# Kernel optimization log

Measured on AMD Instinct MI355X. Metric: run time of the kernel, lower is better.

Reference implementation:

```python
import jax, jax.numpy as jnp
import numpy as np

N_NODES = 50000
N_EDGES = 800000
EPS = 0.1

def setup_inputs() -> dict:
    key = jax.random.key(0)
    ks = jax.random.split(key, 6)
    x = jax.random.normal(ks[0], (N_NODES, 256), dtype=jnp.float32)
    edge_index = jax.random.randint(ks[1], (2, N_EDGES), 0, N_NODES, dtype=jnp.int64)
    W1 = jax.random.normal(ks[2], (256, 64), dtype=jnp.float32) * (1.0 / np.sqrt(256))
    b1 = jnp.zeros((64,), dtype=jnp.float32)
    att = jax.random.normal(ks[3], (2, 1, 64), dtype=jnp.float32) * (1.0 / np.sqrt(64))
    W2 = jax.random.normal(ks[4], (64, 16), dtype=jnp.float32) * (1.0 / np.sqrt(64))
    b2 = jnp.zeros((16,), dtype=jnp.float32)
    return {"x": x, "edge_index": edge_index, "W1": W1, "b1": b1, "att": att, "W2": W2, "b2": b2}

def _fagcn_conv(x, row, col, norm, att_l, eps):
    # message: norm * x_j gathered at source (row), scatter-add to target (col)
    msg = norm[:, None] * x[row]                      # [E_tot, H]
    x_l = jax.ops.segment_sum(msg, col, num_segments=N_NODES)  # low-pass
    x_h = -eps * x_l                                   # high-pass message = -eps * low message
    gate = jax.nn.sigmoid(jnp.sum(x * att_l, axis=-1, keepdims=True))  # [N,1]
    return gate * x_l + (1.0 - gate) * x_h

def reference(x, edge_index, W1, b1, att, W2, b2):
    # add self loops once (same edge set is reused by every layer)
    loops = jnp.arange(N_NODES, dtype=edge_index.dtype)
    row = jnp.concatenate([edge_index[0], loops])
    col = jnp.concatenate([edge_index[1], loops])
    deg = jax.ops.segment_sum(jnp.ones_like(col, dtype=x.dtype), col, num_segments=N_NODES)
    dinv = jnp.where(deg > 0, jax.lax.rsqrt(jnp.maximum(deg, 1e-30)), 0.0)
    norm = dinv[row] * dinv[col]                       # [E_tot]
    # eval mode: dropout is identity
    h = jax.nn.relu(x @ W1 + b1)                       # [N, H]
    for l in range(att.shape[0]):
        h = _fagcn_conv(h, row, col, norm, att[l], EPS)
    return h @ W2 + b2                                 # [N, out]
```

## Files before the change

### kernel.cpp

```cpp
#include <hip/hip_runtime.h>
#include <math.h>

#define N_FEAT_IN 256
#define N_HID 64
#define N_OUT 16
#define EPS 0.1f

typedef short bf16x8 __attribute__((ext_vector_type(8)));
typedef float f32x4 __attribute__((ext_vector_type(4)));

__device__ inline uint pack2(ushort a, ushort b) { return (uint)a | ((uint)b << 16); }

__device__ inline ushort bf16_rne(float x) {
    uint b = __float_as_uint(x);
    b += 0x7fff + ((b >> 16) & 1);
    return (ushort)(b >> 16);
}

__device__ inline float blo(uint u) { return __uint_as_float(u << 16); }
__device__ inline float bhi(uint u) { return __uint_as_float(u & 0xffff0000u); }

__device__ inline void split_bf16(float x, ushort& hi, ushort& lo) {
    uint b = __float_as_uint(x);
    hi = (ushort)(b >> 16);
    float xl = x - __uint_as_float(b & 0xffff0000u);
    lo = (ushort)(__float_as_uint(xl) >> 16);
}


__global__ void zero_int(int* __restrict__ p, int n) {
    int i = blockIdx.x * blockDim.x + threadIdx.x;
    if (i < n) p[i] = 0;
}


__global__ void hist_rank(const int* __restrict__ col, int* __restrict__ cnt,
                          int* __restrict__ rank, int E) {
    int e = blockIdx.x * blockDim.x + threadIdx.x;
    if (e < E) rank[e] = atomicAdd(&cnt[col[e]], 1);
}


__global__ void scan_chunks(const int* __restrict__ cnt, int* __restrict__ rowptr,
                            int* __restrict__ partial, float* __restrict__ dinv, int N) {
    __shared__ int sm[256];
    int tid = threadIdx.x;
    int gid = blockIdx.x * 256 + tid;
    int v = (gid < N) ? cnt[gid] : 0;
    sm[tid] = v;
    __syncthreads();
#pragma unroll
    for (int off = 1; off < 256; off <<= 1) {
        int add = (tid >= off) ? sm[tid - off] : 0;
        __syncthreads();
        sm[tid] += add;
        __syncthreads();
    }
    if (gid < N) {
        rowptr[gid] = sm[tid] - v;
        dinv[gid] = rsqrtf(1.0f + (float)v);
    }
    if (tid == 255) partial[blockIdx.x] = sm[255];
}

__global__ void scan_partials(int* __restrict__ partial, int nchunks) {
    __shared__ int sm[256];
    int tid = threadIdx.x;
    int v = (tid < nchunks) ? partial[tid] : 0;
    sm[tid] = v;
    __syncthreads();
#pragma unroll
    for (int off = 1; off < 256; off <<= 1) {
        int add = (tid >= off) ? sm[tid - off] : 0;
        __syncthreads();
        sm[tid] += add;
        __syncthreads();
    }
    if (tid < nchunks) partial[tid] = sm[tid] - v;
}

__global__ void scan_finish(int* __restrict__ rowptr, const int* __restrict__ partial,
                            int N, int E) {
    int gid = blockIdx.x * 256 + threadIdx.x;
    if (gid < N) rowptr[gid] += partial[blockIdx.x];
    if (gid == 0) rowptr[N] = E;
}


__global__ void csr_scatter_part(const int* __restrict__ row, const int* __restrict__ col,
                                 const int* __restrict__ rank, const int* __restrict__ rowptr,
                                 ushort* __restrict__ srcidx, int E, int rangeSz) {
    int r = blockIdx.x & 7;
    int nsl = gridDim.x >> 3;
    int s = blockIdx.x >> 3;
    int lo = r * rangeSz;
    int hi = lo + rangeSz;
    int stride = nsl * blockDim.x;
    for (int e = s * blockDim.x + threadIdx.x; e < E; e += stride) {
        int c = col[e];
        if (c >= lo && c < hi) {
            srcidx[rowptr[c] + rank[e]] = (ushort)row[e];
        }
    }
}


__global__ __launch_bounds__(256) void gemm1_mfma(const float* __restrict__ x,
                                                  const float* __restrict__ W1,
                                                  const float* __restrict__ b1,
                                                  const float* __restrict__ dinv,
                                                  uint* __restrict__ AsOut,
                                                  int MB, int totalWaves) {
    __shared__ uint4 wh_lds[2048];
    __shared__ uint4 wl_lds[2048];
    int tid = threadIdx.x;
    for (int e = tid; e < 2048; e += 256) {
        int ks = e >> 8;
        int rem = e & 255;
        int nt = rem >> 6;
        int ln = rem & 63;
        int k0 = ks * 32 + ((ln >> 4) << 3);
        int colw = nt * 16 + (ln & 15);
        ushort hi[8], lo[8];
#pragma unroll
        for (int i = 0; i < 8; ++i) {
            float v = W1[(k0 + i) * 64 + colw];
            split_bf16(v, hi[i], lo[i]);
        }
        wh_lds[e] = make_uint4(pack2(hi[0], hi[1]), pack2(hi[2], hi[3]),
                               pack2(hi[4], hi[5]), pack2(hi[6], hi[7]));
        wl_lds[e] = make_uint4(pack2(lo[0], lo[1]), pack2(lo[2], lo[3]),
                               pack2(lo[4], lo[5]), pack2(lo[6], lo[7]));
    }
    __syncthreads();

    int lane = tid & 63;
    int m = lane & 15;
    int kg = lane >> 4;
    int wid = blockIdx.x * 4 + (tid >> 6);
    const bf16x8* whf = reinterpret_cast<const bf16x8*>(wh_lds);
    const bf16x8* wlf = reinterpret_cast<const bf16x8*>(wl_lds);
    float bias[4];
#pragma unroll
    for (int nt = 0; nt < 4; ++nt) bias[nt] = b1[nt * 16 + m];

    auto load_tile = [&](float4* dst, int mbv) {
        const float4* xr = reinterpret_cast<const float4*>(x) +
                           (size_t)(mbv * 16 + m) * 64 + kg * 2;
#pragma unroll
        for (int ks = 0; ks < 8; ++ks) {
            dst[2 * ks]     = xr[ks * 8];
            dst[2 * ks + 1] = xr[ks * 8 + 1];
        }
    };

    int mb = wid;
    if (mb >= MB) return;
    float4 xv[16], xn[16];
    load_tile(xv, mb);

    while (true) {
        int mbn = mb + totalWaves;
        bool has_next = (mbn < MB);
        if (has_next) load_tile(xn, mbn);

        f32x4 acc[4] = {{0.f,0.f,0.f,0.f},{0.f,0.f,0.f,0.f},
                        {0.f,0.f,0.f,0.f},{0.f,0.f,0.f,0.f}};
#pragma unroll
        for (int ks = 0; ks < 8; ++ks) {
            float4 a0 = xv[2 * ks];
            float4 a1 = xv[2 * ks + 1];
            float f[8] = {a0.x, a0.y, a0.z, a0.w, a1.x, a1.y, a1.z, a1.w};
            bf16x8 ah, al;
#pragma unroll
            for (int i = 0; i < 8; ++i) {
                ushort hu, lu;
                split_bf16(f[i], hu, lu);
                ah[i] = (short)hu;
                al[i] = (short)lu;
            }
#pragma unroll
            for (int nt = 0; nt < 4; ++nt) {
                bf16x8 wh = whf[(ks * 4 + nt) * 64 + lane];
                bf16x8 wl = wlf[(ks * 4 + nt) * 64 + lane];
                acc[nt] = __builtin_amdgcn_mfma_f32_16x16x32_bf16(ah, wh, acc[nt], 0, 0, 0);
                acc[nt] = __builtin_amdgcn_mfma_f32_16x16x32_bf16(al, wh, acc[nt], 0, 0, 0);
                acc[nt] = __builtin_amdgcn_mfma_f32_16x16x32_bf16(ah, wl, acc[nt], 0, 0, 0);
            }
        }

        int r0 = mb * 16 + kg * 4;
        float dr[4];
#pragma unroll
        for (int j = 0; j < 4; ++j) dr[j] = dinv[r0 + j];
#pragma unroll
        for (int nt = 0; nt < 4; ++nt) {
#pragma unroll
            for (int j = 0; j < 4; ++j) {
                float v = fmaxf(acc[nt][j] + bias[nt], 0.0f) * dr[j];
                float p = __shfl_xor(v, 1, 64);
                if ((m & 1) == 0) {
                    uint u = pack2(bf16_rne(v), bf16_rne(p));
                    AsOut[(size_t)(r0 + j) * 32 + ((nt * 16 + m) >> 1)] = u;
                }
            }
        }

        if (!has_next) break;
#pragma unroll
        for (int u = 0; u < 16; ++u) xv[u] = xn[u];
        mb = mbn;
    }
}


template <bool LAST>
__global__ __launch_bounds__(256) void fagcn_layer(
    const uint2* __restrict__ As2, uint2* __restrict__ Out2,
    const float* __restrict__ dinv, const int* __restrict__ rowptr,
    const ushort* __restrict__ src, const float* __restrict__ att_l,
    const float* __restrict__ W2, const float* __restrict__ b2,
    float* __restrict__ out, int N) {
    __shared__ float W2s[64 * 16];
    __shared__ float hL[16 * 68];
    int tid = threadIdx.x;
    if (LAST) {
        for (int e = tid; e < 64 * 16; e += 256) W2s[e] = W2[e];
        __syncthreads();
    }
    int sub = tid & 15;
    int lnode = tid >> 4;
    int i = blockIdx.x * 16 + lnode;
    if (i >= N) i = N - 1;

    int start = rowptr[i];
    int end = rowptr[i + 1];
    uint2 su = As2[(size_t)i * 16 + sub];
    float self0 = blo(su.x), self1 = bhi(su.x);
    float self2 = blo(su.y), self3 = bhi(su.y);

    float aA0 = 0.f, aA1 = 0.f, aA2 = 0.f, aA3 = 0.f;
    float aB0 = 0.f, aB1 = 0.f, aB2 = 0.f, aB3 = 0.f;
    int j = start;
    for (; j + 3 < end; j += 4) {
        int s0 = src[j];
        int s1 = src[j + 1];
        int s2 = src[j + 2];
        int s3 = src[j + 3];
        uint2 u0 = As2[(size_t)s0 * 16 + sub];
        uint2 u1 = As2[(size_t)s1 * 16 + sub];
        uint2 u2 = As2[(size_t)s2 * 16 + sub];
        uint2 u3 = As2[(size_t)s3 * 16 + sub];
        aA0 += blo(u0.x); aA1 += bhi(u0.x); aA2 += blo(u0.y); aA3 += bhi(u0.y);
        aB0 += blo(u1.x); aB1 += bhi(u1.x); aB2 += blo(u1.y); aB3 += bhi(u1.y);
        aA0 += blo(u2.x); aA1 += bhi(u2.x); aA2 += blo(u2.y); aA3 += bhi(u2.y);
        aB0 += blo(u3.x); aB1 += bhi(u3.x); aB2 += blo(u3.y); aB3 += bhi(u3.y);
    }
    for (; j < end; ++j) {
        int s = src[j];
        uint2 u = As2[(size_t)s * 16 + sub];
        aA0 += blo(u.x); aA1 += bhi(u.x); aA2 += blo(u.y); aA3 += bhi(u.y);
    }
    float acc0 = aA0 + aB0, acc1 = aA1 + aB1;
    float acc2 = aA2 + aB2, acc3 = aA3 + aB3;

    float d = dinv[i];
    float4 at = reinterpret_cast<const float4*>(att_l)[sub];
    float prod = self0 * at.x + self1 * at.y + self2 * at.z + self3 * at.w;
#pragma unroll
    for (int off = 8; off > 0; off >>= 1)
        prod += __shfl_xor(prod, off, 64);
    float gate = 1.0f / (1.0f + expf(-prod / d));
    float factor = gate * (1.0f + EPS) - EPS;
    float h0 = d * (acc0 + self0) * factor;
    float h1 = d * (acc1 + self1) * factor;
    float h2 = d * (acc2 + self2) * factor;
    float h3 = d * (acc3 + self3) * factor;

    if (!LAST) {
        Out2[(size_t)i * 16 + sub] =
            make_uint2(pack2(bf16_rne(d * h0), bf16_rne(d * h1)),
                       pack2(bf16_rne(d * h2), bf16_rne(d * h3)));
    } else {
        float* hrow = &hL[lnode * 68];
        hrow[4 * sub + 0] = h0;
        hrow[4 * sub + 1] = h1;
        hrow[4 * sub + 2] = h2;
        hrow[4 * sub + 3] = h3;
        __syncthreads();
        const float4* h4 = reinterpret_cast<const float4*>(hrow);
        float acc = b2[sub];
#pragma unroll
        for (int k4 = 0; k4 < 16; ++k4) {
            float4 hv = h4[k4];
            int k = 4 * k4;
            acc = fmaf(hv.x, W2s[(k + 0) * 16 + sub], acc);
            acc = fmaf(hv.y, W2s[(k + 1) * 16 + sub], acc);
            acc = fmaf(hv.z, W2s[(k + 2) * 16 + sub], acc);
            acc = fmaf(hv.w, W2s[(k + 3) * 16 + sub], acc);
        }
        out[(size_t)i * 16 + sub] = acc;
    }
}

extern "C" void kernel_launch(void* const* d_in, const int* in_sizes, int n_in,
                              void* d_out, int out_size, void* d_ws, size_t ws_size,
                              hipStream_t stream) {
    const float* x   = (const float*)d_in[0];
    const int*   ei  = (const int*)d_in[1];
    const float* W1  = (const float*)d_in[2];
    const float* b1  = (const float*)d_in[3];
    const float* att = (const float*)d_in[4];
    const float* W2  = (const float*)d_in[5];
    const float* b2  = (const float*)d_in[6];
    float* out = (float*)d_out;

    const int N = in_sizes[0] / N_FEAT_IN;
    const int E = in_sizes[1] / 2;
    const int L = in_sizes[4] / N_HID;

    const int* row = ei;
    const int* col = ei + E;

    char* wp = (char*)d_ws;
    auto alloc = [&](size_t bytes) -> char* {
        char* p = wp;
        wp += (bytes + 255) & ~(size_t)255;
        return p;
    };
    float*  dinv    = (float*)alloc((size_t)N * 4);
    int*    cnt     = (int*)alloc((size_t)N * 4);
    int*    rowptr  = (int*)alloc((size_t)(N + 1) * 4);
    int*    rank    = (int*)alloc((size_t)E * 4);
    int*    partial = (int*)alloc(256 * 4);
    ushort* srcidx  = (ushort*)alloc((size_t)E * 2);
    uint*   AsA     = (uint*)alloc((size_t)N * 32 * 4);
    uint*   AsB     = (uint*)alloc((size_t)N * 32 * 4);

    const int TB = 256;
    const int nchunks = (N + TB - 1) / TB;
    const int rangeSz = (N + 7) / 8;
    const int PART_GRID = 1024;

    zero_int<<<(N + TB - 1) / TB, TB, 0, stream>>>(cnt, N);
    hist_rank<<<(E + TB - 1) / TB, TB, 0, stream>>>(col, cnt, rank, E);
    scan_chunks<<<nchunks, TB, 0, stream>>>(cnt, rowptr, partial, dinv, N);
    scan_partials<<<1, TB, 0, stream>>>(partial, nchunks);
    scan_finish<<<nchunks, TB, 0, stream>>>(rowptr, partial, N, E);
    csr_scatter_part<<<PART_GRID, TB, 0, stream>>>(row, col, rank, rowptr, srcidx, E, rangeSz);

    {
        const int blocks = 512;
        const int MB = N / 16;
        gemm1_mfma<<<blocks, TB, 0, stream>>>(x, W1, b1, dinv, AsA, MB, blocks * 4);
    }

    {
        int grid = (N + 15) / 16;
        uint2* A = (uint2*)AsA;
        uint2* B = (uint2*)AsB;
        for (int l = 0; l < L; ++l) {
            const float* att_l = att + (size_t)l * N_HID;
            if (l == L - 1) {
                fagcn_layer<true><<<grid, TB, 0, stream>>>(
                    A, B, dinv, rowptr, srcidx, att_l, W2, b2, out, N);
            } else {
                fagcn_layer<false><<<grid, TB, 0, stream>>>(
                    A, B, dinv, rowptr, srcidx, att_l, W2, b2, out, N);
                uint2* tmp = A; A = B; B = tmp;
            }
        }
    }
}
```

Baseline: 138.1 us.

## Fuse CSR scatter into GEMM1 launch and widen per-thread gather to 8 features

Merges the CSR scatter kernel and the MFMA GEMM1 kernel into one launch. Odd block groups do the partitioned scatter and even groups do the GEMM, so the two independent stages run concurrently. The FAGCN layer now has 8 threads per node, each loading a uint4 of 8 bf16 features, so every block covers 32 nodes instead of 16. This means wider gather loads and fewer shuffle steps, at the cost of more registers per thread and scatter blocks that still allocate the GEMM's LDS.

```diff
diff --git a/kernel.cpp b/kernel.cpp
--- a/kernel.cpp
+++ b/kernel.cpp
@@ -87,32 +87,33 @@
 }
 
 
-__global__ void csr_scatter_part(const int* __restrict__ row, const int* __restrict__ col,
-                                 const int* __restrict__ rank, const int* __restrict__ rowptr,
-                                 ushort* __restrict__ srcidx, int E, int rangeSz) {
-    int r = blockIdx.x & 7;
-    int nsl = gridDim.x >> 3;
-    int s = blockIdx.x >> 3;
-    int lo = r * rangeSz;
-    int hi = lo + rangeSz;
-    int stride = nsl * blockDim.x;
-    for (int e = s * blockDim.x + threadIdx.x; e < E; e += stride) {
-        int c = col[e];
-        if (c >= lo && c < hi) {
-            srcidx[rowptr[c] + rank[e]] = (ushort)row[e];
-        }
-    }
-}
-
-
-__global__ __launch_bounds__(256) void gemm1_mfma(const float* __restrict__ x,
-                                                  const float* __restrict__ W1,
-                                                  const float* __restrict__ b1,
-                                                  const float* __restrict__ dinv,
-                                                  uint* __restrict__ AsOut,
-                                                  int MB, int totalWaves) {
+__global__ __launch_bounds__(256) void scatter_gemm1(
+    const int* __restrict__ row, const int* __restrict__ col,
+    const int* __restrict__ rank, const int* __restrict__ rowptr,
+    ushort* __restrict__ srcidx, int E, int rangeSz,
+    const float* __restrict__ x, const float* __restrict__ W1,
+    const float* __restrict__ b1, const float* __restrict__ dinv,
+    uint* __restrict__ AsOut, int MB) {
     __shared__ uint4 wh_lds[2048];
     __shared__ uint4 wl_lds[2048];
+
+    int bid = blockIdx.x;
+    int g = bid >> 3;
+    int w = bid & 7;
+
+    if (g & 1) {
+        int s = g >> 1;
+        int nsl = gridDim.x >> 4;
+        int lo = w * rangeSz;
+        int hi = lo + rangeSz;
+        int stride = nsl * 256;
+        for (int e = s * 256 + threadIdx.x; e < E; e += stride) {
+            int c = col[e];
+            if (c >= lo && c < hi) srcidx[rowptr[c] + rank[e]] = (ushort)row[e];
+        }
+        return;
+    }
+
     int tid = threadIdx.x;
     for (int e = tid; e < 2048; e += 256) {
         int ks = e >> 8;
@@ -137,7 +138,9 @@
     int lane = tid & 63;
     int m = lane & 15;
     int kg = lane >> 4;
-    int wid = blockIdx.x * 4 + (tid >> 6);
+    int gblk = (g >> 1) * 8 + w;
+    int totalWaves = (gridDim.x >> 1) * 4;
+    int wid = gblk * 4 + (tid >> 6);
     const bf16x8* whf = reinterpret_cast<const bf16x8*>(wh_lds);
     const bf16x8* wlf = reinterpret_cast<const bf16x8*>(wl_lds);
     float bias[4];
@@ -216,90 +219,104 @@
 
 template <bool LAST>
 __global__ __launch_bounds__(256) void fagcn_layer(
-    const uint2* __restrict__ As2, uint2* __restrict__ Out2,
+    const uint4* __restrict__ As4, uint4* __restrict__ Out4,
     const float* __restrict__ dinv, const int* __restrict__ rowptr,
     const ushort* __restrict__ src, const float* __restrict__ att_l,
     const float* __restrict__ W2, const float* __restrict__ b2,
     float* __restrict__ out, int N) {
     __shared__ float W2s[64 * 16];
-    __shared__ float hL[16 * 68];
+    __shared__ float hL[32 * 68];
     int tid = threadIdx.x;
     if (LAST) {
         for (int e = tid; e < 64 * 16; e += 256) W2s[e] = W2[e];
         __syncthreads();
     }
-    int sub = tid & 15;
-    int lnode = tid >> 4;
-    int i = blockIdx.x * 16 + lnode;
+    int sub = tid & 7;
+    int lnode = tid >> 3;
+    int i = blockIdx.x * 32 + lnode;
     if (i >= N) i = N - 1;
 
     int start = rowptr[i];
     int end = rowptr[i + 1];
-    uint2 su = As2[(size_t)i * 16 + sub];
-    float self0 = blo(su.x), self1 = bhi(su.x);
-    float self2 = blo(su.y), self3 = bhi(su.y);
-
-    float aA0 = 0.f, aA1 = 0.f, aA2 = 0.f, aA3 = 0.f;
-    float aB0 = 0.f, aB1 = 0.f, aB2 = 0.f, aB3 = 0.f;
+    uint4 su = As4[(size_t)i * 8 + sub];
+    float s0 = blo(su.x), s1 = bhi(su.x), s2 = blo(su.y), s3 = bhi(su.y);
+    float s4 = blo(su.z), s5 = bhi(su.z), s6 = blo(su.w), s7 = bhi(su.w);
+
+    float aA0=0.f,aA1=0.f,aA2=0.f,aA3=0.f,aA4=0.f,aA5=0.f,aA6=0.f,aA7=0.f;
+    float aB0=0.f,aB1=0.f,aB2=0.f,aB3=0.f,aB4=0.f,aB5=0.f,aB6=0.f,aB7=0.f;
     int j = start;
     for (; j + 3 < end; j += 4) {
-        int s0 = src[j];
-        int s1 = src[j + 1];
-        int s2 = src[j + 2];
-        int s3 = src[j + 3];
-        uint2 u0 = As2[(size_t)s0 * 16 + sub];
-        uint2 u1 = As2[(size_t)s1 * 16 + sub];
-        uint2 u2 = As2[(size_t)s2 * 16 + sub];
-        uint2 u3 = As2[(size_t)s3 * 16 + sub];
+        int e0 = src[j];
+        int e1 = src[j + 1];
+        int e2 = src[j + 2];
+        int e3 = src[j + 3];
+        uint4 u0 = As4[(size_t)e0 * 8 + sub];
+        uint4 u1 = As4[(size_t)e1 * 8 + sub];
+        uint4 u2 = As4[(size_t)e2 * 8 + sub];
+        uint4 u3 = As4[(size_t)e3 * 8 + sub];
         aA0 += blo(u0.x); aA1 += bhi(u0.x); aA2 += blo(u0.y); aA3 += bhi(u0.y);
+        aA4 += blo(u0.z); aA5 += bhi(u0.z); aA6 += blo(u0.w); aA7 += bhi(u0.w);
         aB0 += blo(u1.x); aB1 += bhi(u1.x); aB2 += blo(u1.y); aB3 += bhi(u1.y);
+        aB4 += blo(u1.z); aB5 += bhi(u1.z); aB6 += blo(u1.w); aB7 += bhi(u1.w);
         aA0 += blo(u2.x); aA1 += bhi(u2.x); aA2 += blo(u2.y); aA3 += bhi(u2.y);
+        aA4 += blo(u2.z); aA5 += bhi(u2.z); aA6 += blo(u2.w); aA7 += bhi(u2.w);
         aB0 += blo(u3.x); aB1 += bhi(u3.x); aB2 += blo(u3.y); aB3 += bhi(u3.y);
+        aB4 += blo(u3.z); aB5 += bhi(u3.z); aB6 += blo(u3.w); aB7 += bhi(u3.w);
     }
     for (; j < end; ++j) {
         int s = src[j];
-        uint2 u = As2[(size_t)s * 16 + sub];
+        uint4 u = As4[(size_t)s * 8 + sub];
         aA0 += blo(u.x); aA1 += bhi(u.x); aA2 += blo(u.y); aA3 += bhi(u.y);
-    }
-    float acc0 = aA0 + aB0, acc1 = aA1 + aB1;
-    float acc2 = aA2 + aB2, acc3 = aA3 + aB3;
+        aA4 += blo(u.z); aA5 += bhi(u.z); aA6 += blo(u.w); aA7 += bhi(u.w);
+    }
+    float c0 = aA0 + aB0, c1 = aA1 + aB1, c2 = aA2 + aB2, c3 = aA3 + aB3;
+    float c4 = aA4 + aB4, c5 = aA5 + aB5, c6 = aA6 + aB6, c7 = aA7 + aB7;
 
     float d = dinv[i];
-    float4 at = reinterpret_cast<const float4*>(att_l)[sub];
-    float prod = self0 * at.x + self1 * at.y + self2 * at.z + self3 * at.w;
-#pragma unroll
-    for (int off = 8; off > 0; off >>= 1)
+    float4 at0 = reinterpret_cast<const float4*>(att_l)[2 * sub];
+    float4 at1 = reinterpret_cast<const float4*>(att_l)[2 * sub + 1];
+    float prod = s0 * at0.x + s1 * at0.y + s2 * at0.z + s3 * at0.w +
+                 s4 * at1.x + s5 * at1.y + s6 * at1.z + s7 * at1.w;
+#pragma unroll
+    for (int off = 4; off > 0; off >>= 1)
         prod += __shfl_xor(prod, off, 64);
     float gate = 1.0f / (1.0f + expf(-prod / d));
     float factor = gate * (1.0f + EPS) - EPS;
-    float h0 = d * (acc0 + self0) * factor;
-    float h1 = d * (acc1 + self1) * factor;
-    float h2 = d * (acc2 + self2) * factor;
-    float h3 = d * (acc3 + self3) * factor;
+    float df = d * factor;
+    float h0 = df * (c0 + s0), h1 = df * (c1 + s1);
+    float h2 = df * (c2 + s2), h3 = df * (c3 + s3);
+    float h4 = df * (c4 + s4), h5 = df * (c5 + s5);
+    float h6 = df * (c6 + s6), h7 = df * (c7 + s7);
 
     if (!LAST) {
-        Out2[(size_t)i * 16 + sub] =
-            make_uint2(pack2(bf16_rne(d * h0), bf16_rne(d * h1)),
-                       pack2(bf16_rne(d * h2), bf16_rne(d * h3)));
+        Out4[(size_t)i * 8 + sub] =
+            make_uint4(pack2(bf16_rne(d * h0), bf16_rne(d * h1)),
+                       pack2(bf16_rne(d * h2), bf16_rne(d * h3)),
+                       pack2(bf16_rne(d * h4), bf16_rne(d * h5)),
+                       pack2(bf16_rne(d * h6), bf16_rne(d * h7)));
     } else {
-        float* hrow = &hL[lnode * 68];
-        hrow[4 * sub + 0] = h0;
-        hrow[4 * sub + 1] = h1;
-        hrow[4 * sub + 2] = h2;
-        hrow[4 * sub + 3] = h3;
-        __syncthreads();
-        const float4* h4 = reinterpret_cast<const float4*>(hrow);
-        float acc = b2[sub];
+        float4* hrow4 = reinterpret_cast<float4*>(&hL[lnode * 68]);
+        hrow4[2 * sub]     = make_float4(h0, h1, h2, h3);
+        hrow4[2 * sub + 1] = make_float4(h4, h5, h6, h7);
+        __syncthreads();
+        const float4* h4p = reinterpret_cast<const float4*>(&hL[lnode * 68]);
+        float accA = b2[sub];
+        float accB = b2[sub + 8];
 #pragma unroll
         for (int k4 = 0; k4 < 16; ++k4) {
-            float4 hv = h4[k4];
+            float4 hv = h4p[k4];
             int k = 4 * k4;
-            acc = fmaf(hv.x, W2s[(k + 0) * 16 + sub], acc);
-            acc = fmaf(hv.y, W2s[(k + 1) * 16 + sub], acc);
-            acc = fmaf(hv.z, W2s[(k + 2) * 16 + sub], acc);
-            acc = fmaf(hv.w, W2s[(k + 3) * 16 + sub], acc);
-        }
-        out[(size_t)i * 16 + sub] = acc;
+            accA = fmaf(hv.x, W2s[(k + 0) * 16 + sub], accA);
+            accB = fmaf(hv.x, W2s[(k + 0) * 16 + sub + 8], accB);
+            accA = fmaf(hv.y, W2s[(k + 1) * 16 + sub], accA);
+            accB = fmaf(hv.y, W2s[(k + 1) * 16 + sub + 8], accB);
+            accA = fmaf(hv.z, W2s[(k + 2) * 16 + sub], accA);
+            accB = fmaf(hv.z, W2s[(k + 2) * 16 + sub + 8], accB);
+            accA = fmaf(hv.w, W2s[(k + 3) * 16 + sub], accA);
+            accB = fmaf(hv.w, W2s[(k + 3) * 16 + sub + 8], accB);
+        }
+        out[(size_t)i * 16 + sub] = accA;
+        out[(size_t)i * 16 + sub + 8] = accB;
     }
 }
 
@@ -340,25 +357,25 @@
     const int TB = 256;
     const int nchunks = (N + TB - 1) / TB;
     const int rangeSz = (N + 7) / 8;
-    const int PART_GRID = 1024;
 
     zero_int<<<(N + TB - 1) / TB, TB, 0, stream>>>(cnt, N);
     hist_rank<<<(E + TB - 1) / TB, TB, 0, stream>>>(col, cnt, rank, E);
     scan_chunks<<<nchunks, TB, 0, stream>>>(cnt, rowptr, partial, dinv, N);
     scan_partials<<<1, TB, 0, stream>>>(partial, nchunks);
     scan_finish<<<nchunks, TB, 0, stream>>>(rowptr, partial, N, E);
-    csr_scatter_part<<<PART_GRID, TB, 0, stream>>>(row, col, rank, rowptr, srcidx, E, rangeSz);
 
     {
-        const int blocks = 512;
+        const int blocks = 1536;
         const int MB = N / 16;
-        gemm1_mfma<<<blocks, TB, 0, stream>>>(x, W1, b1, dinv, AsA, MB, blocks * 4);
+        scatter_gemm1<<<blocks, TB, 0, stream>>>(row, col, rank, rowptr, srcidx,
+                                                 E, rangeSz,
+                                                 x, W1, b1, dinv, AsA, MB);
     }
 
     {
-        int grid = (N + 15) / 16;
-        uint2* A = (uint2*)AsA;
-        uint2* B = (uint2*)AsB;
+        int grid = (N + 31) / 32;
+        uint4* A = (uint4*)AsA;
+        uint4* B = (uint4*)AsB;
         for (int l = 0; l < L; ++l) {
             const float* att_l = att + (size_t)l * N_HID;
             if (l == L - 1) {
@@ -367,7 +384,7 @@
             } else {
                 fagcn_layer<false><<<grid, TB, 0, stream>>>(
                     A, B, dinv, rowptr, srcidx, att_l, W2, b2, out, N);
-                uint2* tmp = A; A = B; B = tmp;
+                uint4* tmp = A; A = B; B = tmp;
             }
         }
     }
```

New measurement: 203.2 us. 1.47x slower.
